# Optimization experiments

Measured on AMD Instinct MI355X. Metric: run time of the kernel, lower is better.

The kernel has to match this reference:

```python
import jax, jax.numpy as jnp
import numpy as np

C_S = 384
C_Z = 128
C_OUT = 1


def setup_inputs() -> dict:
    key = jax.random.key(0)
    k1, k2, k3 = jax.random.split(key, 3)
    B, N = 1, 1024
    s = jax.random.normal(k1, (B, N, C_S), dtype=jnp.float32)
    z = jax.random.normal(k2, (B, N, N, C_Z), dtype=jnp.float32)
    # Linear(2*c_s + c_z -> c_out); init='final' zeros weights in the original,
    # use small random weights for a meaningful correctness baseline.
    W = jax.random.normal(k3, (C_OUT, 2 * C_S + C_Z), dtype=jnp.float32) * 0.02
    b = jnp.zeros((C_OUT,), dtype=jnp.float32)
    return {"s": s, "z": z, "W": W, "b": b}


def reference(s, z, W, b):
    # Mathematically identical to cat([s_i, s_j, z], -1) @ W.T + b, but
    # decomposed so the (B,N,N,2*c_s+c_z) intermediate is never materialized.
    Wi = W[:, :C_S]            # weights hitting s_i (broadcast over j)
    Wj = W[:, C_S:2 * C_S]     # weights hitting s_j (broadcast over i)
    Wz = W[:, 2 * C_S:]        # weights hitting z
    si = jnp.einsum('bnd,od->bno', s, Wi)          # [B,N,c_out]
    sj = jnp.einsum('bnd,od->bno', s, Wj)          # [B,N,c_out]
    zz = jnp.einsum('bnmc,oc->bnmo', z, Wz)        # [B,N,N,c_out]
    logits = si[:, :, None, :] + sj[:, None, :, :] + zz + b
    return logits
```

## Files before the change

kernel.cpp:

```cpp
#include <hip/hip_runtime.h>

#define C_S 384
#define C_Z 128
#define N_SEQ 1024

__global__ __launch_bounds__(256) void sisj_kernel(const float* __restrict__ s,
                                                   const float* __restrict__ W,
                                                   const float* __restrict__ b,
                                                   float* __restrict__ si,
                                                   float* __restrict__ sj) {
    const int lane = threadIdx.x & 63;
    const int wave = threadIdx.x >> 6;
    const int n = blockIdx.x * 4 + wave;

    const float* srow = s + (size_t)n * C_S;
    const float* Wi = W;
    const float* Wj = W + C_S;

    float acc_i = 0.f, acc_j = 0.f;
#pragma unroll
    for (int j = 0; j < C_S / 64; ++j) {
        const int idx = lane + 64 * j;
        const float v = srow[idx];
        acc_i += v * Wi[idx];
        acc_j += v * Wj[idx];
    }
#pragma unroll
    for (int mask = 32; mask >= 1; mask >>= 1) {
        acc_i += __shfl_xor(acc_i, mask);
        acc_j += __shfl_xor(acc_j, mask);
    }
    if (lane == 0) {
        si[n] = acc_i;
        sj[n] = acc_j + b[0];
    }
}

__global__ __launch_bounds__(256) void contact_kernel(const float* __restrict__ z,
                                                      const float* __restrict__ W,
                                                      const float* __restrict__ si,
                                                      const float* __restrict__ sj,
                                                      float* __restrict__ out) {
    const int lane = threadIdx.x & 63;
    const int wave = threadIdx.x >> 6;
    const int half = lane >> 5;
    const int l = lane & 31;
    const long long gw = (long long)blockIdx.x * 4 + wave;
    const long long o = gw * 2 + half;

    const float4 wz = *(const float4*)(W + 2 * C_S + 4 * l);

    const float4 z4 = *(const float4*)(z + (o << 7) + 4 * l);

    float p = z4.x * wz.x + z4.y * wz.y + z4.z * wz.z + z4.w * wz.w;

#pragma unroll
    for (int mask = 16; mask >= 1; mask >>= 1) {
        p += __shfl_xor(p, mask);
    }

    if (l == 0) {
        const int n = (int)(o >> 10);
        const int m = (int)(o & 1023);
        out[o] = p + si[n] + sj[m];
    }
}

extern "C" void kernel_launch(void* const* d_in, const int* in_sizes, int n_in,
                              void* d_out, int out_size, void* d_ws, size_t ws_size,
                              hipStream_t stream) {
    const float* s = (const float*)d_in[0];
    const float* z = (const float*)d_in[1];
    const float* W = (const float*)d_in[2];
    const float* b = (const float*)d_in[3];
    float* out = (float*)d_out;

    float* si = (float*)d_ws;
    float* sj = si + N_SEQ;

    sisj_kernel<<<N_SEQ / 4, 256, 0, stream>>>(s, W, b, si, sj);

    const int total_outputs = N_SEQ * N_SEQ;
    const int blocks = total_outputs / (2 * 4);
    contact_kernel<<<blocks, 256, 0, stream>>>(z, W, si, sj, out);
}
```

Measured before the change: 674.8 us.

## Use persistent grid-stride waves processing multiple pairs with batched loads

Replaces the one-pair-per-half-wave launch of over a hundred thousand blocks with a fixed grid of persistent blocks. Each wave loops over chunks of eight output pairs, issuing eight float4 loads before reducing. The goal is to raise memory-level parallelism and amortize block scheduling overhead on a bandwidth-bound reduction. The cost is higher register use and a fixed grid size that may underfill or imbalance the device.

```diff
diff --git a/kernel.cpp b/kernel.cpp
--- a/kernel.cpp
+++ b/kernel.cpp
@@ -36,6 +36,9 @@
     }
 }
 
+#define U_PAIRS 8
+#define CONTACT_BLOCKS 2048
+
 __global__ __launch_bounds__(256) void contact_kernel(const float* __restrict__ z,
                                                       const float* __restrict__ W,
                                                       const float* __restrict__ si,
@@ -45,24 +48,46 @@
     const int wave = threadIdx.x >> 6;
     const int half = lane >> 5;
     const int l = lane & 31;
-    const long long gw = (long long)blockIdx.x * 4 + wave;
-    const long long o = gw * 2 + half;
+    const int gw = blockIdx.x * 4 + wave;
+    const int nwaves = CONTACT_BLOCKS * 4;
 
     const float4 wz = *(const float4*)(W + 2 * C_S + 4 * l);
 
-    const float4 z4 = *(const float4*)(z + (o << 7) + 4 * l);
+    const int NPAIRS = (N_SEQ * N_SEQ) / 2;
+    const int NCHUNK = NPAIRS / U_PAIRS;
 
-    float p = z4.x * wz.x + z4.y * wz.y + z4.z * wz.z + z4.w * wz.w;
+    for (int c = gw; c < NCHUNK; c += nwaves) {
+        const float* zb = z + (size_t)c * (U_PAIRS * 256) + 4 * lane;
+
+        float4 z4[U_PAIRS];
+#pragma unroll
+        for (int u = 0; u < U_PAIRS; ++u) {
+            z4[u] = *(const float4*)(zb + u * 256);
+        }
+
+        float p[U_PAIRS];
+#pragma unroll
+        for (int u = 0; u < U_PAIRS; ++u) {
+            p[u] = z4[u].x * wz.x + z4[u].y * wz.y + z4[u].z * wz.z + z4[u].w * wz.w;
+        }
 
 #pragma unroll
-    for (int mask = 16; mask >= 1; mask >>= 1) {
-        p += __shfl_xor(p, mask);
-    }
+        for (int mask = 16; mask >= 1; mask >>= 1) {
+#pragma unroll
+            for (int u = 0; u < U_PAIRS; ++u) {
+                p[u] += __shfl_xor(p[u], mask);
+            }
+        }
 
-    if (l == 0) {
-        const int n = (int)(o >> 10);
-        const int m = (int)(o & 1023);
-        out[o] = p + si[n] + sj[m];
+        if (l == 0) {
+#pragma unroll
+            for (int u = 0; u < U_PAIRS; ++u) {
+                const long long o = (((long long)c * U_PAIRS + u) << 1) + half;
+                const int n = (int)(o >> 10);
+                const int m = (int)(o & 1023);
+                out[o] = p[u] + si[n] + sj[m];
+            }
+        }
     }
 }
 
@@ -80,7 +105,5 @@
 
     sisj_kernel<<<N_SEQ / 4, 256, 0, stream>>>(s, W, b, si, sj);
 
-    const int total_outputs = N_SEQ * N_SEQ;
-    const int blocks = total_outputs / (2 * 4);
-    contact_kernel<<<blocks, 256, 0, stream>>>(z, W, si, sj, out);
+    contact_kernel<<<CONTACT_BLOCKS, 256, 0, stream>>>(z, W, si, sj, out);
 }
```

After: 683.4 us. Within noise of the previous version (+1.3%).
